# Performance work log

Hardware: AMD Instinct MI355X
Metric: run time of the kernel (lower is better)

The kernel has to match this reference:

```python
import jax, jax.numpy as jnp
import numpy as np
from jax import lax

E, C, N = 3, 2, 2048          # edge types, channels, nodes (= nb_items)
B, T = 64, 50                 # batch, max_seq_length
W_IN = 256; W_OUT = 256; U = 512  # gcn in/out, rnn_units


def setup_inputs() -> dict:
    key = jax.random.key(0)
    ks = jax.random.split(key, 16)
    # sparse-ish adjacency stored densely (coalesce/spspmm equivalents are dense ops)
    A = jnp.where(jax.random.uniform(ks[0], (E, N, N)) < 0.01,
                  jax.random.uniform(ks[1], (E, N, N)), 0.0)
    X = jax.random.normal(ks[2], (N, W_IN)) * 0.1
    seqs = (jax.random.uniform(ks[3], (B, T, N)) < 0.005).astype(jnp.float32)  # multi-hot baskets
    seq_len = jax.random.randint(ks[4], (B,), 1, T + 1)
    h0 = jnp.zeros((B, U), jnp.float32)
    c0 = jnp.zeros((B, U), jnp.float32)
    # GTConv weights: init constant 1 (softmax -> uniform filter)
    gt_w1 = jnp.ones((C, E), jnp.float32)
    gt_w2 = jnp.ones((C, E), jnp.float32)
    gt_w3 = jnp.ones((C, E), jnp.float32)
    s_in = 1.0 / np.sqrt(W_IN)
    gcn_W = jax.random.normal(ks[5], (W_IN, W_OUT)) * s_in
    gcn_b = jnp.zeros((W_OUT,), jnp.float32)
    lin1_W = jax.random.normal(ks[6], (C * W_OUT, W_OUT)) * (1.0 / np.sqrt(C * W_OUT))
    lin1_b = jnp.zeros((W_OUT,), jnp.float32)
    s_u = 1.0 / np.sqrt(U)
    lstm_Wih = jax.random.normal(ks[7], (4 * U, W_OUT)) * s_u
    lstm_Whh = jax.random.normal(ks[8], (4 * U, U)) * s_u
    lstm_bih = jnp.zeros((4 * U,), jnp.float32)
    lstm_bhh = jnp.zeros((4 * U,), jnp.float32)
    score_W = jax.random.normal(ks[9], (N, U)) * s_u
    return {"A": A, "X": X, "seqs": seqs, "seq_len": seq_len, "h0": h0, "c0": c0,
            "gt_w1": gt_w1, "gt_w2": gt_w2, "gt_w3": gt_w3,
            "gcn_W": gcn_W, "gcn_b": gcn_b, "lin1_W": lin1_W, "lin1_b": lin1_b,
            "lstm_Wih": lstm_Wih, "lstm_Whh": lstm_Whh,
            "lstm_bih": lstm_bih, "lstm_bhh": lstm_bhh, "score_W": score_W}


def _gtconv(A, w):
    # filter = softmax over edge types; per-channel convex combine of adjacencies
    f = jax.nn.softmax(w, axis=1)            # [C,E]
    return jnp.einsum('ce,enm->cnm', f, A)   # [C,N,N]


def _col_normalize(H):
    # remove self loops; deg = scatter_add over col; value *= deg_col^-1 (no_grad deg)
    H = H * (1.0 - jnp.eye(N, dtype=H.dtype))
    deg = H.sum(axis=1)                      # [C,N] per-column degree
    dinv = lax.stop_gradient(jnp.where(deg > 0, 1.0 / deg, 0.0))
    return H * dinv[:, None, :]


def _gcn(M, X, W, b):
    # PyG GCNConv: add self loops, sym-normalize by col/row degree, aggregate at target
    M1 = M + jnp.eye(N, dtype=M.dtype)
    deg = M1.sum(axis=0)                     # scatter over col
    dis = jnp.where(deg > 0, lax.rsqrt(deg), 0.0)
    Ahat = dis[:, None] * M1 * dis[None, :]
    return Ahat.T @ (X @ W) + b              # out[target] = sum_src norm * x[src]


def reference(A, X, seqs, seq_len, h0, c0, gt_w1, gt_w2, gt_w3,
              gcn_W, gcn_b, lin1_W, lin1_b,
              lstm_Wih, lstm_Whh, lstm_bih, lstm_bhh, score_W):
    # --- GT layers: H = conv1(A) @ conv2(A), then H = norm(H) @ conv(A) ---
    HA = _gtconv(A, gt_w1)
    HB = _gtconv(A, gt_w2)
    H = jnp.einsum('cnk,ckm->cnm', HA, HB)          # spspmm per channel
    Hn = _col_normalize(H)
    HB2 = _gtconv(A, gt_w3)
    H = jnp.einsum('cnk,ckm->cnm', Hn, HB2)
    # --- GCN per channel, relu, concat, linear1 ---
    feats = [jax.nn.relu(_gcn(H[i], X, gcn_W, gcn_b)) for i in range(C)]
    X_ = jnp.concatenate(feats, axis=1) @ lin1_W + lin1_b   # [N, W_OUT]
    # --- basket max-pooling over items in each basket (empty -> zeros) ---
    def pool_step(_, mask_t):                # mask_t: [B,N]
        masked = jnp.where(mask_t[:, :, None] > 0, X_[None, :, :], -jnp.inf)
        pooled = masked.max(axis=1)          # [B, W_OUT]
        has = mask_t.sum(axis=1) > 0
        return None, jnp.where(has[:, None], pooled, 0.0)
    _, bs = lax.scan(pool_step, None, jnp.swapaxes(seqs, 0, 1))  # [T,B,W_OUT]
    # --- single-layer LSTM (PyTorch gate order i,f,g,o) ---
    def lstm_step(carry, x_t):
        h, c = carry
        g = x_t @ lstm_Wih.T + h @ lstm_Whh.T + lstm_bih + lstm_bhh
        i, f, gg, o = jnp.split(g, 4, axis=-1)
        c = jax.nn.sigmoid(f) * c + jax.nn.sigmoid(i) * jnp.tanh(gg)
        h = jax.nn.sigmoid(o) * jnp.tanh(c)
        return (h, c), h
    _, outs = lax.scan(lstm_step, (h0, c0), bs)      # [T,B,U]
    lstm_out = jnp.swapaxes(outs, 0, 1)              # [B,T,U]
    actual = lstm_out[jnp.arange(B), seq_len - 1]    # [B,U] last valid step
    return jax.nn.sigmoid(actual @ score_W.T)        # [B,N]
```

## Files before the change

### kernel.cpp

```cpp
#include <hip/hip_runtime.h>
#include <stdint.h>

#define E_ 3
#define C_ 2
#define N_ 2048
#define B_ 64
#define T_ 50
#define WIN_ 256
#define WOUT_ 256
#define U_ 512
#define BT_ (B_*T_)
#define BTP_ 3328

typedef unsigned short u16;
typedef unsigned int u32;
typedef __bf16 bf16x8 __attribute__((ext_vector_type(8)));
typedef float f32x4 __attribute__((ext_vector_type(4)));

#define NN_ (2048LL*2048LL)

__device__ __forceinline__ float bf2f(u16 u){
  u32 x = ((u32)u) << 16; return __builtin_bit_cast(float, x);
}
__device__ __forceinline__ u16 f2bf(float f){
  u32 x = __builtin_bit_cast(u32, f);
  u32 r = (x + 0x7fffu + ((x >> 16) & 1u)) >> 16;
  return (u16)r;
}

__device__ __forceinline__ void gload16(const u16* g, u16* l){
  __builtin_amdgcn_global_load_lds((const __attribute__((address_space(1))) u32*)g,
                                   (__attribute__((address_space(3))) u32*)l, 16, 0, 0);
}

__global__ void k_prep0(const float* __restrict__ w1, const float* __restrict__ w2,
                        const float* __restrict__ w3, float* __restrict__ filt,
                        const float* __restrict__ bih, const float* __restrict__ bhh,
                        float* __restrict__ bsum, u32* __restrict__ flagv){
  const int i = blockIdx.x*256 + threadIdx.x;
  bsum[i] = bih[i] + bhh[i];
  flagv[i] = 0;
  if(blockIdx.x==0 && threadIdx.x < 3*C_){
    const int t = threadIdx.x;
    const int fi = t / C_, c = t % C_;
    const float* w = (fi==0) ? w1 : ((fi==1) ? w2 : w3);
    float v[E_]; float mx = -3.4e38f;
    for(int e=0;e<E_;e++){ v[e] = w[c*E_+e]; mx = fmaxf(mx, v[e]); }
    float s = 0.f;
    for(int e=0;e<E_;e++){ v[e] = expf(v[e]-mx); s += v[e]; }
    for(int e=0;e<E_;e++) filt[(fi*C_+c)*E_ + e] = v[e]/s;
  }
}

__global__ void k_combineAll3(const float* __restrict__ A, const float* __restrict__ filt,
                              u16* __restrict__ HA, u16* __restrict__ HBt,
                              u16* __restrict__ HB2t){
  __shared__ float te[3][32][33];
  const int ti = blockIdx.x, tj = blockIdx.y;
  const int x = threadIdx.x, y0 = threadIdx.y;
  #pragma unroll
  for(int i=0;i<4;i++){
    const int y = y0 + i*8;
    const long base = (long)(tj*32+y)*N_ + ti*32 + x;
    const float a0 = A[0*NN_+base], a1 = A[1*NN_+base], a2 = A[2*NN_+base];
    te[0][y][x]=a0; te[1][y][x]=a1; te[2][y][x]=a2;
    #pragma unroll
    for(int c=0;c<C_;c++)
      HA[c*NN_ + base] = f2bf(filt[c*E_]*a0 + filt[c*E_+1]*a1 + filt[c*E_+2]*a2);
  }
  __syncthreads();
  #pragma unroll
  for(int i=0;i<4;i++){
    const int y = y0 + i*8;
    const long ob = (long)(ti*32+y)*N_ + tj*32 + x;
    const float a0=te[0][x][y], a1=te[1][x][y], a2=te[2][x][y];
    #pragma unroll
    for(int c=0;c<C_;c++){
      HBt[c*NN_+ob]  = f2bf(filt[(C_+c)*E_]*a0   + filt[(C_+c)*E_+1]*a1   + filt[(C_+c)*E_+2]*a2);
      HB2t[c*NN_+ob] = f2bf(filt[(2*C_+c)*E_]*a0 + filt[(2*C_+c)*E_+1]*a1 + filt[(2*C_+c)*E_+2]*a2);
    }
  }
}

template<int MODE>
__global__ __launch_bounds__(256) void gemm_bt(
    const u16* __restrict__ Ag, const u16* __restrict__ Bg, void* __restrict__ Cg,
    int K, int ldc, long sA, long sB, long sC,
    const float* __restrict__ disv, int sDis, const float* __restrict__ bias)
{
  __shared__ u16 At[2][128*64];
  __shared__ u16 Bt[2][128*64];
  const int tid = threadIdx.x;
  const int w = tid >> 6, l = tid & 63;
  const int z = blockIdx.z;
  const u16* Ab = Ag + (long)z*sA;
  const u16* Bb = Bg + (long)z*sB;
  const int rowBase = blockIdx.y*128;
  const int colBase = blockIdx.x*128;

  f32x4 acc[4][4];
  #pragma unroll
  for(int i=0;i<4;i++)
    #pragma unroll
    for(int j=0;j<4;j++)
      acc[i][j] = f32x4{0.f,0.f,0.f,0.f};

  const int wr = w >> 1, wc = w & 1;
  const int srow = l >> 3;
  const int scol = ((l & 7) ^ srow) << 3;
  const int frow = l & 15;
  const int fkc = l >> 4;

  const int nk = K >> 6;
  #pragma unroll
  for(int r=0;r<4;r++){
    const int ch = w*4 + r;
    gload16(Ab + (long)(rowBase + ch*8 + srow)*K + scol, &At[0][ch*512]);
    gload16(Bb + (long)(colBase + ch*8 + srow)*K + scol, &Bt[0][ch*512]);
  }
  __syncthreads();

  for(int kt=0; kt<nk; ++kt){
    const int cur = kt & 1;
    if(kt+1 < nk){
      const int k0 = (kt+1) << 6;
      #pragma unroll
      for(int r=0;r<4;r++){
        const int ch = w*4 + r;
        gload16(Ab + (long)(rowBase + ch*8 + srow)*K + k0 + scol, &At[cur^1][ch*512]);
        gload16(Bb + (long)(colBase + ch*8 + srow)*K + k0 + scol, &Bt[cur^1][ch*512]);
      }
    }
    #pragma unroll
    for(int ks=0; ks<2; ++ks){
      bf16x8 af[4], bfv[4];
      #pragma unroll
      for(int m=0;m<4;m++){
        const int rr = wr*64 + m*16 + frow;
        af[m] = *(const bf16x8*)&At[cur][rr*64 + (((ks*4 + fkc) ^ (rr&7))<<3)];
      }
      #pragma unroll
      for(int n=0;n<4;n++){
        const int rr = wc*64 + n*16 + frow;
        bfv[n] = *(const bf16x8*)&Bt[cur][rr*64 + (((ks*4 + fkc) ^ (rr&7))<<3)];
      }
      #pragma unroll
      for(int m=0;m<4;m++)
        #pragma unroll
        for(int n=0;n<4;n++)
          acc[m][n] = __builtin_amdgcn_mfma_f32_16x16x32_bf16(af[m], bfv[n], acc[m][n], 0, 0, 0);
    }
    if(kt+1 < nk) __syncthreads();
  }

  #pragma unroll
  for(int m=0;m<4;m++){
    const int row0 = rowBase + wr*64 + m*16 + (l>>4)*4;
    #pragma unroll
    for(int n=0;n<4;n++){
      const int col = colBase + wc*64 + n*16 + (l&15);
      #pragma unroll
      for(int r=0;r<4;r++){
        const float v = acc[m][n][r];
        if(MODE==1){
          ((u16*)Cg)[z*sC + (long)(row0+r)*ldc + col] = f2bf(v);
        } else if(MODE==2){
          float o = disv[z*(long)sDis + row0 + r]*v + bias[col];
          o = o > 0.f ? o : 0.f;
          ((u16*)Cg)[z*sC + (long)(row0+r)*ldc + col] = f2bf(o);
        } else if(MODE==3){
          ((float*)Cg)[z*sC + (long)(row0+r)*ldc + col] = v + bias[col];
        } else if(MODE==4){
          const int row = row0 + r;
          if(row < BT_){
            const int bb = row/50, tt = row - bb*50;
            const int gate = col >> 9, ugg = col & 511;
            ((float*)Cg)[((((long)tt*4 + (bb>>4))*512 + ugg)*16 + (bb&15))*4 + gate] = v + bias[col];
          }
        } else if(MODE==5){
          const int row = row0 + r;
          const float o = (v + (row==col ? 1.f : 0.f)) * disv[z*(long)sDis + col];
          ((u16*)Cg)[z*sC + (long)row*ldc + col] = f2bf(o);
        } else if(MODE==6){
          const int row = row0 + r;
          if(row < B_)
            ((float*)Cg)[(long)row*ldc + col] = 1.f/(1.f + expf(-v));
        }
      }
    }
  }
}

__global__ void k_degpart(const u16* __restrict__ H, float* __restrict__ partial){
  const int c = blockIdx.z;
  const int col = blockIdx.x*256 + threadIdx.x;
  const int r0 = blockIdx.y*128;
  const u16* Hc = H + c*NN_;
  float s = 0.f;
  #pragma unroll 4
  for(int r=0;r<128;r++) s += bf2f(Hc[(long)(r0+r)*N_ + col]);
  partial[((long)c*16 + blockIdx.y)*N_ + col] = s;
}

__global__ void k_dinv(const u16* __restrict__ H, const float* __restrict__ partial,
                       float* __restrict__ dinvb){
  const int i = blockIdx.x*256 + threadIdx.x;
  const int c = i >> 11, m = i & (N_-1);
  float s = 0.f;
  #pragma unroll
  for(int p=0;p<16;p++) s += partial[((long)c*16 + p)*N_ + m];
  s -= bf2f(H[c*NN_ + (long)m*N_ + m]);
  dinvb[i] = s > 0.f ? 1.f/s : 0.f;
}

__global__ void k_colscale(u16* __restrict__ H, const float* __restrict__ dinvb){
  const long i = (long)blockIdx.x*256 + threadIdx.x;
  const int c = blockIdx.y;
  const int j = (int)(i >> 11), ii = (int)(i & (N_-1));
  const long idx = c*NN_ + i;
  const float v = (j==ii) ? 0.f : bf2f(H[idx])*dinvb[c*N_ + ii];
  H[idx] = f2bf(v);
}

__global__ void k_dis(const u16* __restrict__ HB2t, const float* __restrict__ dinvb,
                      float* __restrict__ disv){
  const int c = blockIdx.y, j = blockIdx.x;
  const u16* r = HB2t + (c*(long)N_ + j)*N_;
  const float* dv = dinvb + c*N_;
  float s = 0.f;
  for(int i=threadIdx.x;i<N_;i+=256)
    if(dv[i] > 0.f) s += bf2f(r[i]);
  __shared__ float red[256];
  red[threadIdx.x] = s;
  __syncthreads();
  for(int st=128; st>0; st>>=1){
    if(threadIdx.x < st) red[threadIdx.x] += red[threadIdx.x+st];
    __syncthreads();
  }
  if(threadIdx.x==0){
    const float deg = red[0] + 1.f;
    disv[c*N_ + j] = deg > 0.f ? rsqrtf(deg) : 0.f;
  }
}

__global__ void k_transpose3(const float* __restrict__ gcnW, u16* __restrict__ Wt,
                             const float* __restrict__ lin1W, u16* __restrict__ l1Wt){
  const float* in; u16* out; int R, Cc;
  if(blockIdx.z==0){ in=gcnW;  out=Wt;   R=WIN_;     Cc=WOUT_; }
  else { in=lin1W; out=l1Wt; R=C_*WOUT_; Cc=WOUT_; }
  const int ti = blockIdx.x, tj = blockIdx.y;
  if(ti >= (Cc>>5) || tj >= (R>>5)) return;
  __shared__ float tt[32][33];
  const int x = threadIdx.x, y0 = threadIdx.y;
  #pragma unroll
  for(int i=0;i<4;i++){
    const int y = y0 + i*8;
    tt[y][x] = in[(long)(tj*32+y)*Cc + ti*32 + x];
  }
  __syncthreads();
  #pragma unroll
  for(int i=0;i<4;i++){
    const int y = y0 + i*8;
    out[(long)(ti*32+y)*R + tj*32 + x] = f2bf(tt[x][y]);
  }
}

__global__ void k_cast3(const float* __restrict__ X, u16* __restrict__ Xbf,
                        const float* __restrict__ Wih, u16* __restrict__ Wihbf,
                        const float* __restrict__ scoreW, u16* __restrict__ sWbf){
  const long i = (long)blockIdx.x*256 + threadIdx.x;
  if(i < (long)N_*WIN_) Xbf[i] = f2bf(X[i]);
  else if(i < (long)N_*WIN_ + 4*U_*WOUT_){
    const long j = i - (long)N_*WIN_; Wihbf[j] = f2bf(Wih[j]);
  } else {
    const long j = i - (long)N_*WIN_ - 4*U_*WOUT_; sWbf[j] = f2bf(scoreW[j]);
  }
}

__global__ void k_pool(const float* __restrict__ seqs, const float* __restrict__ X_,
                       u16* __restrict__ bs){
  const int t = blockIdx.x, b = blockIdx.y;
  const int f = threadIdx.x;
  if(t >= T_){
    bs[(long)(BT_ + b*2 + (t-T_))*WOUT_ + f] = 0;
    return;
  }
  const float* mask = seqs + ((long)b*T_ + t)*N_;
  __shared__ int list[N_];
  __shared__ int cnt;
  if(f==0) cnt = 0;
  __syncthreads();
  for(int n0=f; n0<N_; n0+=256){
    if(mask[n0] > 0.f){
      int p = atomicAdd(&cnt, 1);
      list[p] = n0;
    }
  }
  __syncthreads();
  const int m = cnt;
  float mx = -3.4e38f;
  for(int i=0;i<m;i++)
    mx = fmaxf(mx, X_[(long)list[i]*WOUT_ + f]);
  bs[((long)b*T_ + t)*WOUT_ + f] = f2bf(m>0 ? mx : 0.f);
}

__global__ void k_packWhh3(const float* __restrict__ Whh, u16* __restrict__ P,
                           const float* __restrict__ h0, u16* __restrict__ Hglob){
  const long idx = (long)blockIdx.x*256 + threadIdx.x;
  const int e  = (int)(idx & 7);
  const int kk = (int)((idx >> 3) & 15);
  const int l  = (int)((idx >> 7) & 63);
  const int w  = (int)((idx >> 13) & 7);
  const int s  = (int)(idx >> 16);
  const int lr = w*16 + (l & 15);
  const int gam = lr & 3, ui = lr >> 2;
  const int grow = gam*512 + s*32 + ui;
  const int k = kk*32 + (l >> 4)*8 + e;
  P[idx] = f2bf(Whh[(long)grow*512 + k]);
  if(idx < 32768){
    const int b = (int)(idx >> 9), u = (int)(idx & 511);
    const int grp = b >> 4, bl = b & 15;
    Hglob[grp*16384 + (bl << 9) + (u ^ ((bl & 7) << 3))] = f2bf(h0[idx]);
  }
}

__global__ __launch_bounds__(512) void k_lstm_all(
    const u16* __restrict__ WhhP, const float* __restrict__ Gq,
    const float* __restrict__ c0v, const int* __restrict__ seqlen,
    u16* __restrict__ Hglob, u32* __restrict__ flagv, u16* __restrict__ act)
{
  __shared__ u16 Hl[16*512];
  const int tid = threadIdx.x;
  const int w = tid >> 6, l = tid & 63;
  const int grp = blockIdx.x & 3, s = blockIdx.x >> 2;
  const int fr = l & 15, hi = l >> 4;

  bf16x8 wreg[16];
  const u16* wp = WhhP + (((long)s*8 + w)*64 + l)*128;
  #pragma unroll
  for(int kk=0; kk<16; ++kk)
    wreg[kk] = *(const bf16x8*)&wp[kk*8];

  const int ug = s*32 + w*4 + hi;
  const int bl = fr;
  const int bg = grp*16 + bl;
  float cst = c0v[bg*U_ + ug];
  const int sl = seqlen[bg] - 1;
  u16* Hbase = Hglob + grp*16384;
  const int hswz = (bl & 7) << 3;
  const int fi = (grp*16 + fr)*32;
  const long gqbase = (((long)grp*512 + ug)*16 + bl)*4;
  float4 gq_nxt = *(const float4*)&Gq[gqbase];

  for(int t=0; t<T_; ++t){
    const float4 gq = gq_nxt;
    const u16* Hin = Hbase + (t & 1)*8192;
    #pragma unroll
    for(int r=0; r<2; ++r)
      gload16(Hin + (r*8 + w)*512 + l*8, &Hl[(r*8 + w)*512]);
    __syncthreads();

    f32x4 acc = f32x4{0.f,0.f,0.f,0.f};
    #pragma unroll
    for(int kk=0; kk<16; ++kk){
      const int ke = kk*32 + hi*8;
      bf16x8 bb = *(const bf16x8*)&Hl[(bl << 9) + (ke ^ hswz)];
      acc = __builtin_amdgcn_mfma_f32_16x16x32_bf16(wreg[kk], bb, acc, 0, 0, 0);
    }

    if(t+1 < T_)
      gq_nxt = *(const float4*)&Gq[(long)(t+1)*(4*2048*16) + gqbase];

    const float a0 = acc[0] + gq.x;
    const float a1 = acc[1] + gq.y;
    const float a2 = acc[2] + gq.z;
    const float a3 = acc[3] + gq.w;
    const float ig = 1.f/(1.f + expf(-a0));
    const float fg = 1.f/(1.f + expf(-a1));
    const float gg = tanhf(a2);
    const float og = 1.f/(1.f + expf(-a3));
    cst = fg*cst + ig*gg;
    const float h = og*tanhf(cst);
    u16* Hout = Hbase + ((t+1) & 1)*8192;
    Hout[(bl << 9) + (ug ^ hswz)] = f2bf(h);
    if(sl == t) act[bg*U_ + ug] = f2bf(h);

    if(t == T_-1) break;
    __syncthreads();
    if(tid == 0)
      __hip_atomic_store(&flagv[(grp*16 + s)*32], (u32)(t+1),
                         __ATOMIC_RELEASE, __HIP_MEMORY_SCOPE_AGENT);
    if(w == 0){
      while(__hip_atomic_load(&flagv[fi], __ATOMIC_ACQUIRE,
                              __HIP_MEMORY_SCOPE_AGENT) <= (u32)t){
        __builtin_amdgcn_s_sleep(1);
      }
    }
    __syncthreads();
  }
}

extern "C" void kernel_launch(void* const* d_in, const int* in_sizes, int n_in,
                              void* d_out, int out_size, void* d_ws, size_t ws_size,
                              hipStream_t stream){
  (void)in_sizes; (void)n_in; (void)out_size; (void)ws_size;
  const float* A      = (const float*)d_in[0];
  const float* X      = (const float*)d_in[1];
  const float* seqs   = (const float*)d_in[2];
  const int*   seqlen = (const int*)d_in[3];
  const float* h0     = (const float*)d_in[4];
  const float* c0     = (const float*)d_in[5];
  const float* gtw1   = (const float*)d_in[6];
  const float* gtw2   = (const float*)d_in[7];
  const float* gtw3   = (const float*)d_in[8];
  const float* gcnW   = (const float*)d_in[9];
  const float* gcnB   = (const float*)d_in[10];
  const float* lin1W  = (const float*)d_in[11];
  const float* lin1B  = (const float*)d_in[12];
  const float* Wih    = (const float*)d_in[13];
  const float* Whh    = (const float*)d_in[14];
  const float* bihp   = (const float*)d_in[15];
  const float* bhhp   = (const float*)d_in[16];
  const float* scoreW = (const float*)d_in[17];

  char* ws = (char*)d_ws;
  u16* buf0 = (u16*)(ws + 0);
  u16* buf1 = (u16*)(ws + 16777216);
  u16* buf2 = (u16*)(ws + 33554432);
  char* S0  = ws + 50331648;
  float* filt  = (float*)(S0 + 0);
  float* disv  = (float*)(S0 + 1024);
  u16*  Wt     = (u16*) (S0 + 17408);
  u16*  XWt    = (u16*) (S0 + 148480);
  u16*  catb   = (u16*) (S0 + 1197056);
  u16*  l1Wt   = (u16*) (S0 + 3294208);
  float* Xo    = (float*)(S0 + 3556352);
  u16*  bs     = (u16*) (S0 + 5653504);
  u16*  act    = (u16*) (S0 + 7357440);
  u16*  sWbf   = (u16*) (S0 + 7488512);
  u16*  WhhB   = (u16*) (S0 + 9585664);
  u16*  Xbf    = (u16*) (S0 + 11682816);
  u16*  Wihbf  = (u16*) (S0 + 12731392);
  float* bsum  = (float*)(S0 + 13779968);
  u16*  Hglob  = (u16*) (S0 + 13788160);
  u32*  flagv  = (u32*) (S0 + 13919232);
  float* degp  = (float*)(S0 + 14050304);
  float* dinvb = (float*)(S0 + 14312448);
  u16* buf3 = (u16*)(ws + 64660480);
  u16* HA   = buf0;
  u16* HBt  = buf1;
  u16* Hb   = buf2;
  u16* HB2t = buf3;
  u16* Pd   = buf1;
  float* Gq = (float*)ws;

  k_prep0<<<dim3(8), 256, 0, stream>>>(gtw1, gtw2, gtw3, filt, bihp, bhhp, bsum, flagv);
  k_combineAll3<<<dim3(N_/32, N_/32), dim3(32,8), 0, stream>>>(A, filt, HA, HBt, HB2t);
  k_transpose3<<<dim3(16, 64, 2), dim3(32,8), 0, stream>>>(gcnW, Wt, lin1W, l1Wt);
  k_cast3<<<dim3(8192), 256, 0, stream>>>(X, Xbf, Wih, Wihbf, scoreW, sWbf);
  gemm_bt<1><<<dim3(16,16,C_), 256, 0, stream>>>(HA, HBt, Hb, N_, N_, NN_, NN_, NN_, nullptr, 0, nullptr);
  k_degpart<<<dim3(8, 16, C_), 256, 0, stream>>>(Hb, degp);
  k_dinv<<<dim3(16), 256, 0, stream>>>(Hb, degp, dinvb);
  k_colscale<<<dim3(NN_/256, C_), 256, 0, stream>>>(Hb, dinvb);
  k_dis<<<dim3(N_, C_), 256, 0, stream>>>(HB2t, dinvb, disv);
  gemm_bt<5><<<dim3(16,16,C_), 256, 0, stream>>>(HB2t, Hb, Pd, N_, N_, NN_, NN_, NN_, disv, N_, nullptr);
  gemm_bt<1><<<dim3(N_/128, WOUT_/128, 1), 256, 0, stream>>>(Wt, Xbf, XWt, WIN_, N_, 0, 0, 0, nullptr, 0, nullptr);
  gemm_bt<2><<<dim3(WOUT_/128, N_/128, C_), 256, 0, stream>>>(Pd, XWt, catb, N_, C_*WOUT_, NN_, 0, WOUT_, disv, N_, gcnB);
  gemm_bt<3><<<dim3(WOUT_/128, N_/128, 1), 256, 0, stream>>>(catb, l1Wt, Xo, C_*WOUT_, WOUT_, 0, 0, 0, nullptr, 0, lin1B);
  k_pool<<<dim3(52, B_), 256, 0, stream>>>(seqs, Xo, bs);
  gemm_bt<4><<<dim3((4*U_)/128, BTP_/128, 1), 256, 0, stream>>>(bs, Wihbf, Gq, WOUT_, 0, 0, 0, 0, nullptr, 0, bsum);
  k_packWhh3<<<dim3(4096), 256, 0, stream>>>(Whh, WhhB, h0, Hglob);
  k_lstm_all<<<dim3(64), 512, 0, stream>>>(WhhB, Gq, c0, seqlen, Hglob, flagv, act);
  gemm_bt<6><<<dim3(N_/128, 1, 1), 256, 0, stream>>>(act, sWbf, (float*)d_out, U_, N_, 0, 0, 0, nullptr, 0, nullptr);
}
```

Baseline: 504.0 us.

## Split-K the GCN propagation GEMM and merge small launches

The Pd×XWt GEMM, which launched only 2×16×2 = 64 blocks with K=2048, is split four ways along K (MODE 7). Partial results go to a float scratch buffer, and a new reduction kernel then applies the disv scaling, bias and ReLU. The cast kernel is folded into k_prep0, k_colscale and k_dis are merged into one launch, and the k_pool mask scan uses float4 loads. The goal is better CU occupancy and fewer launches, at the cost of extra scratch traffic and an additional reduction kernel.

```diff
diff --git a/kernel.cpp b/kernel.cpp
--- a/kernel.cpp
+++ b/kernel.cpp
@@ -36,13 +36,26 @@
 __global__ void k_prep0(const float* __restrict__ w1, const float* __restrict__ w2,
                         const float* __restrict__ w3, float* __restrict__ filt,
                         const float* __restrict__ bih, const float* __restrict__ bhh,
-                        float* __restrict__ bsum, u32* __restrict__ flagv){
-  const int i = blockIdx.x*256 + threadIdx.x;
+                        float* __restrict__ bsum, u32* __restrict__ flagv,
+                        const float* __restrict__ X, u16* __restrict__ Xbf,
+                        const float* __restrict__ Wih, u16* __restrict__ Wihbf,
+                        const float* __restrict__ scoreW, u16* __restrict__ sWbf){
+  const long bx = blockIdx.x;
+  if(bx < 8192){
+    const long i = bx*256 + threadIdx.x;
+    if(i < (long)N_*WIN_) Xbf[i] = f2bf(X[i]);
+    else if(i < (long)N_*WIN_ + 4*U_*WOUT_){
+      const long j = i - (long)N_*WIN_; Wihbf[j] = f2bf(Wih[j]);
+    } else {
+      const long j = i - (long)N_*WIN_ - 4*U_*WOUT_; sWbf[j] = f2bf(scoreW[j]);
+    }
+    return;
+  }
+  const int i = (int)(bx - 8192)*256 + threadIdx.x;
   bsum[i] = bih[i] + bhh[i];
   flagv[i] = 0;
-  if(blockIdx.x==0 && threadIdx.x < 3*C_){
-    const int t = threadIdx.x;
-    const int fi = t / C_, c = t % C_;
+  if(i < 3*C_){
+    const int fi = i / C_, c = i % C_;
     const float* w = (fi==0) ? w1 : ((fi==1) ? w2 : w3);
     float v[E_]; float mx = -3.4e38f;
     for(int e=0;e<E_;e++){ v[e] = w[c*E_+e]; mx = fmaxf(mx, v[e]); }
@@ -93,7 +106,9 @@
   const int tid = threadIdx.x;
   const int w = tid >> 6, l = tid & 63;
   const int z = blockIdx.z;
-  const u16* Ab = Ag + (long)z*sA;
+  const int zc = (MODE==7) ? (z >> 2) : z;
+  const int kBase = (MODE==7) ? ((z & 3)*sDis) : 0;
+  const u16* Ab = Ag + (long)zc*sA;
   const u16* Bb = Bg + (long)z*sB;
   const int rowBase = blockIdx.y*128;
   const int colBase = blockIdx.x*128;
@@ -111,19 +126,19 @@
   const int frow = l & 15;
   const int fkc = l >> 4;
 
-  const int nk = K >> 6;
+  const int nk = (MODE==7) ? (sDis >> 6) : (K >> 6);
   #pragma unroll
   for(int r=0;r<4;r++){
     const int ch = w*4 + r;
-    gload16(Ab + (long)(rowBase + ch*8 + srow)*K + scol, &At[0][ch*512]);
-    gload16(Bb + (long)(colBase + ch*8 + srow)*K + scol, &Bt[0][ch*512]);
+    gload16(Ab + (long)(rowBase + ch*8 + srow)*K + kBase + scol, &At[0][ch*512]);
+    gload16(Bb + (long)(colBase + ch*8 + srow)*K + kBase + scol, &Bt[0][ch*512]);
   }
   __syncthreads();
 
   for(int kt=0; kt<nk; ++kt){
     const int cur = kt & 1;
     if(kt+1 < nk){
-      const int k0 = (kt+1) << 6;
+      const int k0 = kBase + ((kt+1) << 6);
       #pragma unroll
       for(int r=0;r<4;r++){
         const int ch = w*4 + r;
@@ -185,10 +200,26 @@
           const int row = row0 + r;
           if(row < B_)
             ((float*)Cg)[(long)row*ldc + col] = 1.f/(1.f + expf(-v));
+        } else if(MODE==7){
+          ((float*)Cg)[((long)z*N_ + row0 + r)*WOUT_ + col] = v;
         }
       }
     }
   }
+}
+
+__global__ void k_catred(const float* __restrict__ P, const float* __restrict__ disv,
+                         const float* __restrict__ gcnB, u16* __restrict__ catb){
+  const int idx = blockIdx.x*256 + threadIdx.x;
+  const int row = idx >> 9;
+  const int cf  = idx & 511;
+  const int c = cf >> 8, f = cf & 255;
+  float s = 0.f;
+  #pragma unroll
+  for(int ks=0;ks<4;ks++)
+    s += P[(((long)(c*4+ks)*N_ + row)<<8) + f];
+  float o = disv[c*N_ + row]*s + gcnB[f];
+  catb[(long)row*(C_*WOUT_) + cf] = f2bf(o > 0.f ? o : 0.f);
 }
 
 __global__ void k_degpart(const u16* __restrict__ H, float* __restrict__ partial){
@@ -213,18 +244,18 @@
   dinvb[i] = s > 0.f ? 1.f/s : 0.f;
 }
 
-__global__ void k_colscale(u16* __restrict__ H, const float* __restrict__ dinvb){
-  const long i = (long)blockIdx.x*256 + threadIdx.x;
+__global__ void k_colscale_dis(u16* __restrict__ H, const float* __restrict__ dinvb,
+                               const u16* __restrict__ HB2t, float* __restrict__ disv){
   const int c = blockIdx.y;
-  const int j = (int)(i >> 11), ii = (int)(i & (N_-1));
-  const long idx = c*NN_ + i;
-  const float v = (j==ii) ? 0.f : bf2f(H[idx])*dinvb[c*N_ + ii];
-  H[idx] = f2bf(v);
-}
-
-__global__ void k_dis(const u16* __restrict__ HB2t, const float* __restrict__ dinvb,
-                      float* __restrict__ disv){
-  const int c = blockIdx.y, j = blockIdx.x;
+  if(blockIdx.x < 16384){
+    const long i = (long)blockIdx.x*256 + threadIdx.x;
+    const int j = (int)(i >> 11), ii = (int)(i & (N_-1));
+    const long idx = c*NN_ + i;
+    const float v = (j==ii) ? 0.f : bf2f(H[idx])*dinvb[c*N_ + ii];
+    H[idx] = f2bf(v);
+    return;
+  }
+  const int j = blockIdx.x - 16384;
   const u16* r = HB2t + (c*(long)N_ + j)*N_;
   const float* dv = dinvb + c*N_;
   float s = 0.f;
@@ -265,18 +296,6 @@
   }
 }
 
-__global__ void k_cast3(const float* __restrict__ X, u16* __restrict__ Xbf,
-                        const float* __restrict__ Wih, u16* __restrict__ Wihbf,
-                        const float* __restrict__ scoreW, u16* __restrict__ sWbf){
-  const long i = (long)blockIdx.x*256 + threadIdx.x;
-  if(i < (long)N_*WIN_) Xbf[i] = f2bf(X[i]);
-  else if(i < (long)N_*WIN_ + 4*U_*WOUT_){
-    const long j = i - (long)N_*WIN_; Wihbf[j] = f2bf(Wih[j]);
-  } else {
-    const long j = i - (long)N_*WIN_ - 4*U_*WOUT_; sWbf[j] = f2bf(scoreW[j]);
-  }
-}
-
 __global__ void k_pool(const float* __restrict__ seqs, const float* __restrict__ X_,
                        u16* __restrict__ bs){
   const int t = blockIdx.x, b = blockIdx.y;
@@ -290,10 +309,16 @@
   __shared__ int cnt;
   if(f==0) cnt = 0;
   __syncthreads();
-  for(int n0=f; n0<N_; n0+=256){
-    if(mask[n0] > 0.f){
-      int p = atomicAdd(&cnt, 1);
-      list[p] = n0;
+  {
+    const float4 m0 = *(const float4*)&mask[f*8];
+    const float4 m1 = *(const float4*)&mask[f*8+4];
+    const float mv[8] = {m0.x,m0.y,m0.z,m0.w,m1.x,m1.y,m1.z,m1.w};
+    #pragma unroll
+    for(int q=0;q<8;q++){
+      if(mv[q] > 0.f){
+        int p = atomicAdd(&cnt, 1);
+        list[p] = f*8 + q;
+      }
     }
   }
   __syncthreads();
@@ -452,20 +477,21 @@
   u16* Hb   = buf2;
   u16* HB2t = buf3;
   u16* Pd   = buf1;
+  float* Pcat = (float*)ws;
   float* Gq = (float*)ws;
 
-  k_prep0<<<dim3(8), 256, 0, stream>>>(gtw1, gtw2, gtw3, filt, bihp, bhhp, bsum, flagv);
+  k_prep0<<<dim3(8200), 256, 0, stream>>>(gtw1, gtw2, gtw3, filt, bihp, bhhp, bsum, flagv,
+                                          X, Xbf, Wih, Wihbf, scoreW, sWbf);
   k_combineAll3<<<dim3(N_/32, N_/32), dim3(32,8), 0, stream>>>(A, filt, HA, HBt, HB2t);
   k_transpose3<<<dim3(16, 64, 2), dim3(32,8), 0, stream>>>(gcnW, Wt, lin1W, l1Wt);
-  k_cast3<<<dim3(8192), 256, 0, stream>>>(X, Xbf, Wih, Wihbf, scoreW, sWbf);
   gemm_bt<1><<<dim3(16,16,C_), 256, 0, stream>>>(HA, HBt, Hb, N_, N_, NN_, NN_, NN_, nullptr, 0, nullptr);
   k_degpart<<<dim3(8, 16, C_), 256, 0, stream>>>(Hb, degp);
   k_dinv<<<dim3(16), 256, 0, stream>>>(Hb, degp, dinvb);
-  k_colscale<<<dim3(NN_/256, C_), 256, 0, stream>>>(Hb, dinvb);
-  k_dis<<<dim3(N_, C_), 256, 0, stream>>>(HB2t, dinvb, disv);
+  k_colscale_dis<<<dim3(16384 + N_, C_), 256, 0, stream>>>(Hb, dinvb, HB2t, disv);
   gemm_bt<5><<<dim3(16,16,C_), 256, 0, stream>>>(HB2t, Hb, Pd, N_, N_, NN_, NN_, NN_, disv, N_, nullptr);
   gemm_bt<1><<<dim3(N_/128, WOUT_/128, 1), 256, 0, stream>>>(Wt, Xbf, XWt, WIN_, N_, 0, 0, 0, nullptr, 0, nullptr);
-  gemm_bt<2><<<dim3(WOUT_/128, N_/128, C_), 256, 0, stream>>>(Pd, XWt, catb, N_, C_*WOUT_, NN_, 0, WOUT_, disv, N_, gcnB);
+  gemm_bt<7><<<dim3(WOUT_/128, N_/128, C_*4), 256, 0, stream>>>(Pd, XWt, Pcat, N_, 0, NN_, 0, 0, nullptr, 512, nullptr);
+  k_catred<<<dim3(4096), 256, 0, stream>>>(Pcat, disv, gcnB, catb);
   gemm_bt<3><<<dim3(WOUT_/128, N_/128, 1), 256, 0, stream>>>(catb, l1Wt, Xo, C_*WOUT_, WOUT_, 0, 0, 0, nullptr, 0, lin1B);
   k_pool<<<dim3(52, B_), 256, 0, stream>>>(seqs, Xo, bs);
   gemm_bt<4><<<dim3((4*U_)/128, BTP_/128, 1), 256, 0, stream>>>(bs, Wihbf, Gq, WOUT_, 0, 0, 0, 0, nullptr, 0, bsum);
```

Measured after the change: 484.9 us, median of 2. 1.04x faster.
